# Kernel optimization log

Measured on AMD Instinct MI355X. Metric: run time of the kernel, lower is better.

Reference implementation:

```python
import jax, jax.numpy as jnp
import numpy as np

N_NODES = 200_000
N_EDGES = 12_800_000


def setup_inputs() -> dict:
    key = jax.random.key(0)
    k1, k2, k3, k4 = jax.random.split(key, 4)
    x = jax.random.normal(k1, (N_NODES, 2), dtype=jnp.float32)
    edge_index = jax.random.randint(k2, (2, N_EDGES), 0, N_NODES, dtype=jnp.int32)
    # Glorot-ish init for the two GCN linear layers
    W1 = jax.random.normal(k3, (2, 16), dtype=jnp.float32) * 0.5
    b1 = jnp.zeros((16,), dtype=jnp.float32)
    W2 = jax.random.normal(k4, (16, 2), dtype=jnp.float32) * 0.25
    b2 = jnp.zeros((2,), dtype=jnp.float32)
    return {"x": x, "W1": W1, "b1": b1, "W2": W2, "b2": b2, "edge_index": edge_index}


def gcn_conv(x, W, b, src, dst, num_nodes):
    # PyG GCNConv: add self-loops, deg from dst (col), norm = d_src^-1/2 * d_dst^-1/2,
    # out[i] = sum_{j->i} norm_e * (x_j W) + (1/deg_i) * (x_i W) + b
    h = x @ W  # [N, F_out]
    ones = jnp.ones(src.shape[0], dtype=h.dtype)
    deg = jax.ops.segment_sum(ones, dst, num_segments=num_nodes) + 1.0  # +1 self-loop
    dinv = jax.lax.rsqrt(deg)  # [N]
    norm = dinv[src] * dinv[dst]  # [E]
    agg = jax.ops.segment_sum(h[src] * norm[:, None], dst, num_segments=num_nodes)
    # self-loop contribution has norm dinv_i * dinv_i = 1/deg_i
    return agg + h * (1.0 / deg)[:, None] + b


def reference(x, W1, b1, W2, b2, edge_index):
    src, dst = edge_index[0], edge_index[1]
    h = gcn_conv(x, W1, b1, src, dst, N_NODES)
    h = jax.nn.relu(h)
    out = gcn_conv(h, W2, b2, src, dst, N_NODES)
    return out
```

## Files before the change

kernel.cpp:

```cpp
#include <hip/hip_runtime.h>


constexpr int N_NODES = 200000;
constexpr int N_EDGES = 12800000;
constexpr int RANGE_SHIFT = 8;
constexpr int K_BUCKETS = (N_NODES + 255) / 256;
constexpr int SORT_BLOCKS = 2048;
constexpr int CHUNK = N_EDGES / SORT_BLOCKS;
constexpr int SCAN_R = SORT_BLOCKS / 256;
constexpr int CAPB = 18432;


__global__ __launch_bounds__(256) void hist_kernel(const int* __restrict__ dst,
                                                   unsigned* __restrict__ blockHist) {
    __shared__ unsigned h[K_BUCKETS];
    for (int i = threadIdx.x; i < K_BUCKETS; i += 256) h[i] = 0;
    __syncthreads();
    int base = blockIdx.x * CHUNK;
    for (int e = base + threadIdx.x; e < base + CHUNK; e += 256)
        atomicAdd(&h[((unsigned)dst[e]) >> RANGE_SHIFT], 1u);
    __syncthreads();
    unsigned* row = blockHist + (size_t)blockIdx.x * K_BUCKETS;
    for (int i = threadIdx.x; i < K_BUCKETS; i += 256) row[i] = h[i];
}

__global__ __launch_bounds__(256) void scan_perblock_kernel(unsigned* __restrict__ blockHist,
                                                            unsigned* __restrict__ bucketTotal) {
    int b = blockIdx.x, t = threadIdx.x;
    unsigned v[SCAN_R], run = 0;
#pragma unroll
    for (int j = 0; j < SCAN_R; j++) v[j] = blockHist[(size_t)(SCAN_R * t + j) * K_BUCKETS + b];
#pragma unroll
    for (int j = 0; j < SCAN_R; j++) { unsigned tmp = v[j]; v[j] = run; run += tmp; }
    __shared__ unsigned sh[256];
    sh[t] = run;
    __syncthreads();
    for (int off = 1; off < 256; off <<= 1) {
        unsigned add = (t >= off) ? sh[t - off] : 0u;
        __syncthreads();
        sh[t] += add;
        __syncthreads();
    }
    unsigned excl = sh[t] - run;
#pragma unroll
    for (int j = 0; j < SCAN_R; j++)
        blockHist[(size_t)(SCAN_R * t + j) * K_BUCKETS + b] = excl + v[j];
    if (t == 255) bucketTotal[b] = sh[255];
}

__global__ __launch_bounds__(1024) void scan_buckets_kernel(const unsigned* __restrict__ bucketTotal,
                                                            unsigned* __restrict__ bucketStart) {
    __shared__ unsigned sh[1024];
    int t = threadIdx.x;
    unsigned v = (t < K_BUCKETS) ? bucketTotal[t] : 0u;
    sh[t] = v;
    __syncthreads();
    for (int off = 1; off < 1024; off <<= 1) {
        unsigned add = (t >= off) ? sh[t - off] : 0u;
        __syncthreads();
        sh[t] += add;
        __syncthreads();
    }
    if (t < K_BUCKETS) bucketStart[t] = sh[t] - v;
    if (t == K_BUCKETS - 1) bucketStart[K_BUCKETS] = sh[t];
}

__global__ __launch_bounds__(256) void scatter_kernel(const int* __restrict__ src,
                                                      const int* __restrict__ dst,
                                                      const unsigned* __restrict__ blockHist,
                                                      const unsigned* __restrict__ bucketTotal,
                                                      const unsigned* __restrict__ bucketStart,
                                                      unsigned* __restrict__ sorted) {
    __shared__ unsigned s_cur[K_BUCKETS];
    __shared__ int      s_base[K_BUCKETS];
    __shared__ unsigned ssum[256];
    __shared__ unsigned ent[CHUNK];
    __shared__ unsigned short bk[CHUNK];

    int t = threadIdx.x;
    int k = blockIdx.x;
    int base = k * CHUNK;
    const unsigned* row  = blockHist + (size_t)k * K_BUCKETS;
    const unsigned* rowN = blockHist + (size_t)(k + 1) * K_BUCKETS;
    bool last = (k == SORT_BLOCKS - 1);

    unsigned v[4], g0[4], run = 0;
#pragma unroll
    for (int j = 0; j < 4; j++) {
        int idx = 4 * t + j;
        if (idx < K_BUCKETS) {
            unsigned r0 = row[idx];
            unsigned r1 = last ? bucketTotal[idx] : rowN[idx];
            g0[j] = r0;
            v[j]  = r1 - r0;
        } else { g0[j] = 0; v[j] = 0; }
    }
#pragma unroll
    for (int j = 0; j < 4; j++) { unsigned tmp = v[j]; v[j] = run; run += tmp; }
    ssum[t] = run;
    __syncthreads();
    for (int off = 1; off < 256; off <<= 1) {
        unsigned add = (t >= off) ? ssum[t - off] : 0u;
        __syncthreads();
        ssum[t] += add;
        __syncthreads();
    }
    unsigned excl = ssum[t] - run;
#pragma unroll
    for (int j = 0; j < 4; j++) {
        int idx = 4 * t + j;
        if (idx < K_BUCKETS) {
            unsigned st = excl + v[j];
            s_cur[idx]  = st;
            s_base[idx] = (int)(bucketStart[idx] + g0[j]) - (int)st;
        }
    }
    __syncthreads();

    for (int e = base + t; e < base + CHUNK; e += 256) {
        unsigned d = (unsigned)dst[e];
        unsigned s = (unsigned)src[e];
        unsigned b = d >> RANGE_SHIFT;
        unsigned lpos = atomicAdd(&s_cur[b], 1u);
        ent[lpos] = s | ((d & 255u) << 18);
        bk[lpos] = (unsigned short)b;
    }
    __syncthreads();

    for (int i = t; i < CHUNK; i += 256) {
        unsigned b = bk[i];
        sorted[s_base[b] + i] = ent[i];
    }
}

__global__ __launch_bounds__(256) void sortbins_kernel(unsigned* __restrict__ sorted,
                                                       const unsigned* __restrict__ bucketStart,
                                                       unsigned* __restrict__ nodeStart) {
    __shared__ unsigned ent[CAPB];
    __shared__ unsigned hist[256];
    __shared__ unsigned cur[256];
    __shared__ unsigned ssum[256];
    int t = threadIdx.x, b = blockIdx.x;
    int base = (int)bucketStart[b];
    int n = (int)bucketStart[b + 1] - base;
    if (n > CAPB) return;

    hist[t] = 0;
    __syncthreads();
    for (int i = t; i < n; i += 256) {
        unsigned w = sorted[base + i];
        ent[i] = w;
        atomicAdd(&hist[(w >> 18) & 255u], 1u);
    }
    __syncthreads();
    unsigned v = hist[t];
    ssum[t] = v;
    __syncthreads();
    for (int off = 1; off < 256; off <<= 1) {
        unsigned add = (t >= off) ? ssum[t - off] : 0u;
        __syncthreads();
        ssum[t] += add;
        __syncthreads();
    }
    unsigned excl = ssum[t] - v;
    cur[t] = excl;
    int node = (b << RANGE_SHIFT) + t;
    if (node < N_NODES) nodeStart[node] = (unsigned)(base + (int)excl);
    if (b == K_BUCKETS - 1 && t == 0) nodeStart[N_NODES] = bucketStart[K_BUCKETS];
    __syncthreads();
    for (int i = t; i < n; i += 256) {
        unsigned w = ent[i];
        unsigned p = atomicAdd(&cur[(w >> 18) & 255u], 1u);
        sorted[base + (int)p] = w;
    }
}


__global__ __launch_bounds__(256) void node1w_kernel(const float2* __restrict__ x,
                                                     const unsigned* __restrict__ nodeStart,
                                                     float* __restrict__ dinv,
                                                     float2* __restrict__ u) {
    int i = blockIdx.x * 256 + threadIdx.x;
    if (i >= N_NODES) return;
    unsigned deg = nodeStart[i + 1] - nodeStart[i] + 1u;
    float di = rsqrtf((float)deg);
    dinv[i] = di;
    float2 xi = x[i];
    u[i] = make_float2(di * xi.x, di * xi.y);
}

__global__ __launch_bounds__(256) void aggw1_kernel(const unsigned* __restrict__ sorted,
                                                    const unsigned* __restrict__ nodeStart,
                                                    const float2* __restrict__ u,
                                                    const float* __restrict__ dinv,
                                                    const float* __restrict__ W1,
                                                    const float* __restrict__ b1,
                                                    const float* __restrict__ W2,
                                                    float2* __restrict__ g2) {
    int i = blockIdx.x * 4 + (threadIdx.x >> 6);
    if (i >= N_NODES) return;
    int lane = threadIdx.x & 63;
    int e0 = (int)nodeStart[i], e1 = (int)nodeStart[i + 1];
    float ax = 0.f, ay = 0.f;
    for (int k = e0 + lane; k < e1; k += 64) {
        unsigned w = sorted[k];
        float2 v = u[w & 0x3FFFFu];
        ax += v.x; ay += v.y;
    }
#pragma unroll
    for (int off = 32; off; off >>= 1) {
        ax += __shfl_xor(ax, off);
        ay += __shfl_xor(ay, off);
    }
    float di = dinv[i];
    float2 uu = u[i];
    float c0 = di * (ax + uu.x);
    float c1 = di * (ay + uu.y);
    float a0 = 0.f, a1 = 0.f;
    if (lane < 16) {
        float o = fmaxf(c0 * W1[lane] + c1 * W1[16 + lane] + b1[lane], 0.f);
        a0 = o * W2[2 * lane];
        a1 = o * W2[2 * lane + 1];
    }
#pragma unroll
    for (int off = 8; off; off >>= 1) {
        a0 += __shfl_xor(a0, off);
        a1 += __shfl_xor(a1, off);
    }
    if (lane == 0) g2[i] = make_float2(di * a0, di * a1);
}

__global__ __launch_bounds__(256) void aggw2_kernel(const unsigned* __restrict__ sorted,
                                                    const unsigned* __restrict__ nodeStart,
                                                    const float2* __restrict__ g2,
                                                    const float* __restrict__ dinv,
                                                    const float* __restrict__ b2,
                                                    float2* __restrict__ out) {
    int i = blockIdx.x * 4 + (threadIdx.x >> 6);
    if (i >= N_NODES) return;
    int lane = threadIdx.x & 63;
    int e0 = (int)nodeStart[i], e1 = (int)nodeStart[i + 1];
    float ax = 0.f, ay = 0.f;
    for (int k = e0 + lane; k < e1; k += 64) {
        unsigned w = sorted[k];
        float2 v = g2[w & 0x3FFFFu];
        ax += v.x; ay += v.y;
    }
#pragma unroll
    for (int off = 32; off; off >>= 1) {
        ax += __shfl_xor(ax, off);
        ay += __shfl_xor(ay, off);
    }
    if (lane == 0) {
        float di = dinv[i];
        float2 g = g2[i];
        out[i] = make_float2(di * (ax + g.x) + b2[0],
                             di * (ay + g.y) + b2[1]);
    }
}


__global__ __launch_bounds__(256) void fb_deg(const int* __restrict__ dst, int* __restrict__ degi) {
    int e = blockIdx.x * 256 + threadIdx.x;
    if (e < N_EDGES) atomicAdd(&degi[dst[e]], 1);
}
__global__ __launch_bounds__(256) void fb_node1(const float* __restrict__ x, const int* __restrict__ degi,
                                                float* __restrict__ dinv, float2* __restrict__ u) {
    int i = blockIdx.x * 256 + threadIdx.x;
    if (i >= N_NODES) return;
    float di = rsqrtf((float)(degi[i] + 1));
    dinv[i] = di;
    float2 xi = ((const float2*)x)[i];
    u[i] = make_float2(di * xi.x, di * xi.y);
}
__global__ __launch_bounds__(256) void fb_agg(const int* __restrict__ src, const int* __restrict__ dst,
                                              const float2* __restrict__ table, float* __restrict__ acc) {
    int e = blockIdx.x * 256 + threadIdx.x;
    if (e >= N_EDGES) return;
    float2 v = table[src[e]];
    size_t d = dst[e];
    unsafeAtomicAdd(&acc[2 * d], v.x);
    unsafeAtomicAdd(&acc[2 * d + 1], v.y);
}
__global__ __launch_bounds__(256) void fb_node2(const float2* __restrict__ u, const float2* __restrict__ A1,
                                                const float* __restrict__ W1, const float* __restrict__ b1,
                                                const float* __restrict__ W2, const float* __restrict__ dinv,
                                                float2* __restrict__ g2) {
    int i = blockIdx.x * 256 + threadIdx.x;
    if (i >= N_NODES) return;
    float di = dinv[i];
    float2 a = A1[i], uu = u[i];
    float c0 = di * (a.x + uu.x), c1 = di * (a.y + uu.y);
    float a0 = 0.f, a1 = 0.f;
#pragma unroll
    for (int f = 0; f < 16; f++) {
        float o = fmaxf(c0 * W1[f] + c1 * W1[16 + f] + b1[f], 0.f);
        a0 += o * W2[2 * f];
        a1 += o * W2[2 * f + 1];
    }
    g2[i] = make_float2(di * a0, di * a1);
}
__global__ __launch_bounds__(256) void fb_node3(const float2* __restrict__ g2, const float2* __restrict__ A2,
                                                const float* __restrict__ b2, const float* __restrict__ dinv,
                                                float2* __restrict__ out) {
    int i = blockIdx.x * 256 + threadIdx.x;
    if (i >= N_NODES) return;
    float di = dinv[i];
    float2 a = A2[i], g = g2[i];
    out[i] = make_float2(di * (a.x + g.x) + b2[0], di * (a.y + g.y) + b2[1]);
}


extern "C" void kernel_launch(void* const* d_in, const int* in_sizes, int n_in,
                              void* d_out, int out_size, void* d_ws, size_t ws_size,
                              hipStream_t stream) {
    const float* x  = (const float*)d_in[0];
    const float* W1 = (const float*)d_in[1];
    const float* b1 = (const float*)d_in[2];
    const float* W2 = (const float*)d_in[3];
    const float* b2 = (const float*)d_in[4];
    const int* ei   = (const int*)d_in[5];
    const int* src = ei;
    const int* dst = ei + N_EDGES;
    float2* out = (float2*)d_out;

    const size_t need = ((size_t)N_EDGES + (size_t)SORT_BLOCKS * K_BUCKETS + 782 + 784) * 4;

    if (ws_size >= need) {
        unsigned* sorted      = (unsigned*)d_ws;
        unsigned* region      = sorted + N_EDGES;
        unsigned* blockHist   = region;
        unsigned* nodeStart   = region;
        float*    dinv        = (float*)(region + 200004);
        float2*   u           = (float2*)(region + 400004);
        float2*   g2          = (float2*)(region + 800004);
        unsigned* bucketTotal = region + (size_t)SORT_BLOCKS * K_BUCKETS;
        unsigned* bucketStart = bucketTotal + 782;

        hist_kernel<<<SORT_BLOCKS, 256, 0, stream>>>(dst, blockHist);
        scan_perblock_kernel<<<K_BUCKETS, 256, 0, stream>>>(blockHist, bucketTotal);
        scan_buckets_kernel<<<1, 1024, 0, stream>>>(bucketTotal, bucketStart);
        scatter_kernel<<<SORT_BLOCKS, 256, 0, stream>>>(src, dst, blockHist, bucketTotal,
                                                        bucketStart, sorted);
        sortbins_kernel<<<K_BUCKETS, 256, 0, stream>>>(sorted, bucketStart, nodeStart);
        node1w_kernel<<<K_BUCKETS, 256, 0, stream>>>((const float2*)x, nodeStart, dinv, u);
        aggw1_kernel<<<(N_NODES + 3) / 4, 256, 0, stream>>>(sorted, nodeStart, u, dinv,
                                                            W1, b1, W2, g2);
        aggw2_kernel<<<(N_NODES + 3) / 4, 256, 0, stream>>>(sorted, nodeStart, g2, dinv,
                                                            b2, out);
    } else {
        float* ws = (float*)d_ws;
        int*   degi = (int*)ws;
        float* A1   = ws + N_NODES;
        float* A2   = A1 + 2 * (size_t)N_NODES;
        float* dinvF = A2 + 2 * (size_t)N_NODES;
        float2* uF  = (float2*)(dinvF + N_NODES);
        float2* g2F = uF + N_NODES;
        constexpr int EB = (N_EDGES + 255) / 256;
        constexpr int NB = (N_NODES + 255) / 256;
        (void)hipMemsetAsync(degi, 0, 5 * (size_t)N_NODES * sizeof(float), stream);
        fb_deg<<<EB, 256, 0, stream>>>(dst, degi);
        fb_node1<<<NB, 256, 0, stream>>>(x, degi, dinvF, uF);
        fb_agg<<<EB, 256, 0, stream>>>(src, dst, uF, A1);
        fb_node2<<<NB, 256, 0, stream>>>(uF, (const float2*)A1, W1, b1, W2, dinvF, g2F);
        fb_agg<<<EB, 256, 0, stream>>>(src, dst, g2F, A2);
        fb_node3<<<NB, 256, 0, stream>>>(g2F, (const float2*)A2, b2, dinvF, out);
    }
}
```

Measured before the change: 520.2 us.

## Fuse histogram into scatter using fixed-capacity buckets and global atomic cursors

New measurement: 614.1 us. 18.0% more time.

```diff
diff --git a/kernel.cpp b/kernel.cpp
--- a/kernel.cpp
+++ b/kernel.cpp
@@ -7,70 +7,20 @@
 constexpr int K_BUCKETS = (N_NODES + 255) / 256;
 constexpr int SORT_BLOCKS = 2048;
 constexpr int CHUNK = N_EDGES / SORT_BLOCKS;
-constexpr int SCAN_R = SORT_BLOCKS / 256;
-constexpr int CAPB = 18432;
-
-
-__global__ __launch_bounds__(256) void hist_kernel(const int* __restrict__ dst,
-                                                   unsigned* __restrict__ blockHist) {
-    __shared__ unsigned h[K_BUCKETS];
-    for (int i = threadIdx.x; i < K_BUCKETS; i += 256) h[i] = 0;
-    __syncthreads();
-    int base = blockIdx.x * CHUNK;
-    for (int e = base + threadIdx.x; e < base + CHUNK; e += 256)
-        atomicAdd(&h[((unsigned)dst[e]) >> RANGE_SHIFT], 1u);
-    __syncthreads();
-    unsigned* row = blockHist + (size_t)blockIdx.x * K_BUCKETS;
-    for (int i = threadIdx.x; i < K_BUCKETS; i += 256) row[i] = h[i];
-}
-
-__global__ __launch_bounds__(256) void scan_perblock_kernel(unsigned* __restrict__ blockHist,
-                                                            unsigned* __restrict__ bucketTotal) {
-    int b = blockIdx.x, t = threadIdx.x;
-    unsigned v[SCAN_R], run = 0;
-#pragma unroll
-    for (int j = 0; j < SCAN_R; j++) v[j] = blockHist[(size_t)(SCAN_R * t + j) * K_BUCKETS + b];
-#pragma unroll
-    for (int j = 0; j < SCAN_R; j++) { unsigned tmp = v[j]; v[j] = run; run += tmp; }
-    __shared__ unsigned sh[256];
-    sh[t] = run;
-    __syncthreads();
-    for (int off = 1; off < 256; off <<= 1) {
-        unsigned add = (t >= off) ? sh[t - off] : 0u;
-        __syncthreads();
-        sh[t] += add;
-        __syncthreads();
-    }
-    unsigned excl = sh[t] - run;
-#pragma unroll
-    for (int j = 0; j < SCAN_R; j++)
-        blockHist[(size_t)(SCAN_R * t + j) * K_BUCKETS + b] = excl + v[j];
-    if (t == 255) bucketTotal[b] = sh[255];
-}
-
-__global__ __launch_bounds__(1024) void scan_buckets_kernel(const unsigned* __restrict__ bucketTotal,
-                                                            unsigned* __restrict__ bucketStart) {
-    __shared__ unsigned sh[1024];
-    int t = threadIdx.x;
-    unsigned v = (t < K_BUCKETS) ? bucketTotal[t] : 0u;
-    sh[t] = v;
-    __syncthreads();
-    for (int off = 1; off < 1024; off <<= 1) {
-        unsigned add = (t >= off) ? sh[t - off] : 0u;
-        __syncthreads();
-        sh[t] += add;
-        __syncthreads();
-    }
-    if (t < K_BUCKETS) bucketStart[t] = sh[t] - v;
-    if (t == K_BUCKETS - 1) bucketStart[K_BUCKETS] = sh[t];
+constexpr int CAP = 17792;
+constexpr int CAPB = CAP;
+
+
+__global__ __launch_bounds__(256) void zero_kernel(unsigned* __restrict__ p, int n) {
+    int i = blockIdx.x * 256 + threadIdx.x;
+    if (i < n) p[i] = 0u;
 }
 
 __global__ __launch_bounds__(256) void scatter_kernel(const int* __restrict__ src,
                                                       const int* __restrict__ dst,
-                                                      const unsigned* __restrict__ blockHist,
-                                                      const unsigned* __restrict__ bucketTotal,
-                                                      const unsigned* __restrict__ bucketStart,
+                                                      unsigned* __restrict__ gCur,
                                                       unsigned* __restrict__ sorted) {
+    __shared__ unsigned h[K_BUCKETS];
     __shared__ unsigned s_cur[K_BUCKETS];
     __shared__ int      s_base[K_BUCKETS];
     __shared__ unsigned ssum[256];
@@ -78,22 +28,19 @@
     __shared__ unsigned short bk[CHUNK];
 
     int t = threadIdx.x;
-    int k = blockIdx.x;
-    int base = k * CHUNK;
-    const unsigned* row  = blockHist + (size_t)k * K_BUCKETS;
-    const unsigned* rowN = blockHist + (size_t)(k + 1) * K_BUCKETS;
-    bool last = (k == SORT_BLOCKS - 1);
-
-    unsigned v[4], g0[4], run = 0;
+    int base = blockIdx.x * CHUNK;
+    for (int i = t; i < K_BUCKETS; i += 256) h[i] = 0;
+    __syncthreads();
+
+    for (int e = base + t; e < base + CHUNK; e += 256)
+        atomicAdd(&h[((unsigned)dst[e]) >> RANGE_SHIFT], 1u);
+    __syncthreads();
+
+    unsigned v[4], run = 0;
 #pragma unroll
     for (int j = 0; j < 4; j++) {
         int idx = 4 * t + j;
-        if (idx < K_BUCKETS) {
-            unsigned r0 = row[idx];
-            unsigned r1 = last ? bucketTotal[idx] : rowN[idx];
-            g0[j] = r0;
-            v[j]  = r1 - r0;
-        } else { g0[j] = 0; v[j] = 0; }
+        v[j] = (idx < K_BUCKETS) ? h[idx] : 0u;
     }
 #pragma unroll
     for (int j = 0; j < 4; j++) { unsigned tmp = v[j]; v[j] = run; run += tmp; }
@@ -110,9 +57,13 @@
     for (int j = 0; j < 4; j++) {
         int idx = 4 * t + j;
         if (idx < K_BUCKETS) {
-            unsigned st = excl + v[j];
-            s_cur[idx]  = st;
-            s_base[idx] = (int)(bucketStart[idx] + g0[j]) - (int)st;
+            unsigned cnt = (idx < K_BUCKETS) ? (((idx == 4 * t + j)) ? 0u : 0u) : 0u;
+            (void)cnt;
+            unsigned localStart = excl + v[j];
+            unsigned c = h[idx];
+            unsigned old = c ? atomicAdd(&gCur[idx], c) : 0u;
+            s_cur[idx]  = localStart;
+            s_base[idx] = (int)((unsigned)idx * CAP + old) - (int)localStart;
         }
     }
     __syncthreads();
@@ -129,21 +80,23 @@
 
     for (int i = t; i < CHUNK; i += 256) {
         unsigned b = bk[i];
-        sorted[s_base[b] + i] = ent[i];
+        int pos = s_base[b] + i;
+        if (pos < (int)((b + 1u) * CAP)) sorted[pos] = ent[i];
     }
 }
 
 __global__ __launch_bounds__(256) void sortbins_kernel(unsigned* __restrict__ sorted,
-                                                       const unsigned* __restrict__ bucketStart,
-                                                       unsigned* __restrict__ nodeStart) {
+                                                       const unsigned* __restrict__ gCur,
+                                                       unsigned* __restrict__ nodeStart,
+                                                       unsigned* __restrict__ nodeEnd) {
     __shared__ unsigned ent[CAPB];
     __shared__ unsigned hist[256];
     __shared__ unsigned cur[256];
     __shared__ unsigned ssum[256];
     int t = threadIdx.x, b = blockIdx.x;
-    int base = (int)bucketStart[b];
-    int n = (int)bucketStart[b + 1] - base;
-    if (n > CAPB) return;
+    int base = b * CAP;
+    int n = (int)gCur[b];
+    if (n > CAP) n = CAP;
 
     hist[t] = 0;
     __syncthreads();
@@ -165,8 +118,10 @@
     unsigned excl = ssum[t] - v;
     cur[t] = excl;
     int node = (b << RANGE_SHIFT) + t;
-    if (node < N_NODES) nodeStart[node] = (unsigned)(base + (int)excl);
-    if (b == K_BUCKETS - 1 && t == 0) nodeStart[N_NODES] = bucketStart[K_BUCKETS];
+    if (node < N_NODES) {
+        nodeStart[node] = (unsigned)(base + (int)excl);
+        nodeEnd[node]   = (unsigned)(base + (int)(excl + v));
+    }
     __syncthreads();
     for (int i = t; i < n; i += 256) {
         unsigned w = ent[i];
@@ -178,11 +133,12 @@
 
 __global__ __launch_bounds__(256) void node1w_kernel(const float2* __restrict__ x,
                                                      const unsigned* __restrict__ nodeStart,
+                                                     const unsigned* __restrict__ nodeEnd,
                                                      float* __restrict__ dinv,
                                                      float2* __restrict__ u) {
     int i = blockIdx.x * 256 + threadIdx.x;
     if (i >= N_NODES) return;
-    unsigned deg = nodeStart[i + 1] - nodeStart[i] + 1u;
+    unsigned deg = nodeEnd[i] - nodeStart[i] + 1u;
     float di = rsqrtf((float)deg);
     dinv[i] = di;
     float2 xi = x[i];
@@ -191,6 +147,7 @@
 
 __global__ __launch_bounds__(256) void aggw1_kernel(const unsigned* __restrict__ sorted,
                                                     const unsigned* __restrict__ nodeStart,
+                                                    const unsigned* __restrict__ nodeEnd,
                                                     const float2* __restrict__ u,
                                                     const float* __restrict__ dinv,
                                                     const float* __restrict__ W1,
@@ -200,7 +157,7 @@
     int i = blockIdx.x * 4 + (threadIdx.x >> 6);
     if (i >= N_NODES) return;
     int lane = threadIdx.x & 63;
-    int e0 = (int)nodeStart[i], e1 = (int)nodeStart[i + 1];
+    int e0 = (int)nodeStart[i], e1 = (int)nodeEnd[i];
     float ax = 0.f, ay = 0.f;
     for (int k = e0 + lane; k < e1; k += 64) {
         unsigned w = sorted[k];
@@ -232,6 +189,7 @@
 
 __global__ __launch_bounds__(256) void aggw2_kernel(const unsigned* __restrict__ sorted,
                                                     const unsigned* __restrict__ nodeStart,
+                                                    const unsigned* __restrict__ nodeEnd,
                                                     const float2* __restrict__ g2,
                                                     const float* __restrict__ dinv,
                                                     const float* __restrict__ b2,
@@ -239,7 +197,7 @@
     int i = blockIdx.x * 4 + (threadIdx.x >> 6);
     if (i >= N_NODES) return;
     int lane = threadIdx.x & 63;
-    int e0 = (int)nodeStart[i], e1 = (int)nodeStart[i + 1];
+    int e0 = (int)nodeStart[i], e1 = (int)nodeEnd[i];
     float ax = 0.f, ay = 0.f;
     for (int k = e0 + lane; k < e1; k += 64) {
         unsigned w = sorted[k];
@@ -324,30 +282,27 @@
     const int* dst = ei + N_EDGES;
     float2* out = (float2*)d_out;
 
-    const size_t need = ((size_t)N_EDGES + (size_t)SORT_BLOCKS * K_BUCKETS + 782 + 784) * 4;
+    const size_t SORTED_W = (size_t)K_BUCKETS * CAP;
+    const size_t need = (SORTED_W + 1400000 + 800) * 4;
 
     if (ws_size >= need) {
-        unsigned* sorted      = (unsigned*)d_ws;
-        unsigned* region      = sorted + N_EDGES;
-        unsigned* blockHist   = region;
-        unsigned* nodeStart   = region;
-        float*    dinv        = (float*)(region + 200004);
-        float2*   u           = (float2*)(region + 400004);
-        float2*   g2          = (float2*)(region + 800004);
-        unsigned* bucketTotal = region + (size_t)SORT_BLOCKS * K_BUCKETS;
-        unsigned* bucketStart = bucketTotal + 782;
-
-        hist_kernel<<<SORT_BLOCKS, 256, 0, stream>>>(dst, blockHist);
-        scan_perblock_kernel<<<K_BUCKETS, 256, 0, stream>>>(blockHist, bucketTotal);
-        scan_buckets_kernel<<<1, 1024, 0, stream>>>(bucketTotal, bucketStart);
-        scatter_kernel<<<SORT_BLOCKS, 256, 0, stream>>>(src, dst, blockHist, bucketTotal,
-                                                        bucketStart, sorted);
-        sortbins_kernel<<<K_BUCKETS, 256, 0, stream>>>(sorted, bucketStart, nodeStart);
-        node1w_kernel<<<K_BUCKETS, 256, 0, stream>>>((const float2*)x, nodeStart, dinv, u);
-        aggw1_kernel<<<(N_NODES + 3) / 4, 256, 0, stream>>>(sorted, nodeStart, u, dinv,
-                                                            W1, b1, W2, g2);
-        aggw2_kernel<<<(N_NODES + 3) / 4, 256, 0, stream>>>(sorted, nodeStart, g2, dinv,
-                                                            b2, out);
+        unsigned* sorted    = (unsigned*)d_ws;
+        unsigned* nodeStart = sorted + SORTED_W;
+        unsigned* nodeEnd   = nodeStart + 200000;
+        float*    dinv      = (float*)(nodeEnd + 200000);
+        float2*   u         = (float2*)(dinv + 200000);
+        float2*   g2        = u + 200000;
+        unsigned* gCur      = (unsigned*)(g2 + 200000);
+
+        zero_kernel<<<(K_BUCKETS + 255) / 256, 256, 0, stream>>>(gCur, K_BUCKETS);
+        scatter_kernel<<<SORT_BLOCKS, 256, 0, stream>>>(src, dst, gCur, sorted);
+        sortbins_kernel<<<K_BUCKETS, 256, 0, stream>>>(sorted, gCur, nodeStart, nodeEnd);
+        node1w_kernel<<<K_BUCKETS, 256, 0, stream>>>((const float2*)x, nodeStart, nodeEnd,
+                                                     dinv, u);
+        aggw1_kernel<<<(N_NODES + 3) / 4, 256, 0, stream>>>(sorted, nodeStart, nodeEnd, u,
+                                                            dinv, W1, b1, W2, g2);
+        aggw2_kernel<<<(N_NODES + 3) / 4, 256, 0, stream>>>(sorted, nodeStart, nodeEnd, g2,
+                                                            dinv, b2, out);
     } else {
         float* ws = (float*)d_ws;
         int*   degi = (int*)ws;
```
